# Kernel tuning notes

Measured on AMD Instinct MI355X. Metric: run time of the kernel, lower is better.

The kernel has to match this reference:

```python
import jax, jax.numpy as jnp
import numpy as np

ALPHA = 20.0 / 100.0  # dt / tau


def setup_inputs() -> dict:
    key = jax.random.key(0)
    ks = jax.random.split(key, 5)
    T, B, I, N = 1000, 256, 128, 512
    return {
        "x": jax.random.normal(ks[0], (T, B, I), dtype=jnp.float32),
        "h0": jax.random.normal(ks[1], (B, N), dtype=jnp.float32) * 0.3,
        "W_in": jax.random.normal(ks[2], (N, I), dtype=jnp.float32) / np.sqrt(I),
        "b_in": jax.random.normal(ks[3], (N,), dtype=jnp.float32) * 0.01,
        "W_hh": jax.random.normal(ks[4], (N, N), dtype=jnp.float32) / np.sqrt(N),
    }


def reference(x, h0, W_in, b_in, W_hh):
    # Precompute input projection for all steps in one GEMM: [T,B,N]
    xproj = jnp.einsum("tbi,ni->tbn", x, W_in) + b_in

    def step(h, xp_t):
        h_new = jnp.tanh(xp_t + h @ W_hh.T)
        h = h * (1.0 - ALPHA) + h_new * ALPHA
        return h, h

    hidden, output = jax.lax.scan(step, h0, xproj)
    return output, hidden
```

## Files before the change

### kernel.cpp

```cpp
#include <hip/hip_runtime.h>
#include <hip/hip_bf16.h>


typedef __bf16 bf16;
typedef __bf16 bf16x8 __attribute__((ext_vector_type(8)));
typedef float floatx4 __attribute__((ext_vector_type(4)));
typedef unsigned short u16;
typedef u16 u16x4 __attribute__((ext_vector_type(4)));

#define T_STEPS 1000
#define BATCH 256
#define NDIM 512
#define IDIM 128

__global__ void pack_kernel(const float* __restrict__ W_hh,
                            const float* __restrict__ W_in,
                            bf16x8* __restrict__ Whpack,
                            bf16x8* __restrict__ WinHi,
                            bf16x8* __restrict__ WinLo) {
    int e = blockIdx.x * 256 + threadIdx.x;
    if (e < 32768) {
        int g = e >> 10, s = (e >> 6) & 15, lane = e & 63;
        int n = 16 * g + (lane & 15);
        int k = 32 * s + 8 * (lane >> 4);
        const float* src = W_hh + n * 512 + k;
        bf16x8 v;
#pragma unroll
        for (int j = 0; j < 8; j++) v[j] = (bf16)src[j];
        Whpack[e] = v;
    } else {
        int e2 = e - 32768;
        if (e2 < 8192) {
            int g = e2 >> 8, s = (e2 >> 6) & 3, lane = e2 & 63;
            int n = 16 * g + (lane & 15);
            int i = 32 * s + 8 * (lane >> 4);
            const float* src = W_in + n * 128 + i;
            bf16x8 vh, vl;
#pragma unroll
            for (int j = 0; j < 8; j++) {
                float w = src[j];
                bf16 h = (bf16)w;
                vh[j] = h;
                vl[j] = (bf16)(w - (float)h);
            }
            WinHi[e2] = vh;
            WinLo[e2] = vl;
        }
    }
}

__global__ __launch_bounds__(256)
void xproj_kernel(const float* __restrict__ x,
                  const float* __restrict__ b_in,
                  const bf16x8* __restrict__ WinHi,
                  const bf16x8* __restrict__ WinLo,
                  float* __restrict__ out) {
    __shared__ float stg[4][2][16 * 36];
    const int wave = threadIdx.x >> 6, lane = threadIdx.x & 63;
    const int m = lane & 15, q = lane >> 4;
    const long tile0 = ((long)blockIdx.x * 4 + wave) * 2;

    bf16x8 ah[2][4], al[2][4];
#pragma unroll
    for (int tt = 0; tt < 2; tt++) {
        const floatx4* xr = (const floatx4*)(x + ((tile0 + tt) * 16 + m) * IDIM);
#pragma unroll
        for (int s = 0; s < 4; s++) {
            floatx4 w0 = xr[s * 8 + q * 2];
            floatx4 w1 = xr[s * 8 + q * 2 + 1];
#pragma unroll
            for (int j = 0; j < 4; j++) {
                float a0 = w0[j], a1 = w1[j];
                bf16 h0 = (bf16)a0, h1 = (bf16)a1;
                ah[tt][s][j] = h0;
                ah[tt][s][j + 4] = h1;
                al[tt][s][j] = (bf16)(a0 - (float)h0);
                al[tt][s][j + 4] = (bf16)(a1 - (float)h1);
            }
        }
    }

    const int rrow = lane >> 3;
    const int rcol = (lane & 7) * 4;

#pragma unroll 2
    for (int gp = 0; gp < 16; gp++) {
        floatx4 acc[2][2];
#pragma unroll
        for (int tt = 0; tt < 2; tt++)
#pragma unroll
            for (int p = 0; p < 2; p++) acc[tt][p] = (floatx4){0.f, 0.f, 0.f, 0.f};

#pragma unroll
        for (int s = 0; s < 4; s++) {
            bf16x8 bh0 = WinHi[((2 * gp) * 4 + s) * 64 + lane];
            bf16x8 bl0 = WinLo[((2 * gp) * 4 + s) * 64 + lane];
            bf16x8 bh1 = WinHi[((2 * gp + 1) * 4 + s) * 64 + lane];
            bf16x8 bl1 = WinLo[((2 * gp + 1) * 4 + s) * 64 + lane];
#pragma unroll
            for (int tt = 0; tt < 2; tt++) {
                acc[tt][0] = __builtin_amdgcn_mfma_f32_16x16x32_bf16(ah[tt][s], bh0, acc[tt][0], 0, 0, 0);
                acc[tt][0] = __builtin_amdgcn_mfma_f32_16x16x32_bf16(al[tt][s], bh0, acc[tt][0], 0, 0, 0);
                acc[tt][0] = __builtin_amdgcn_mfma_f32_16x16x32_bf16(ah[tt][s], bl0, acc[tt][0], 0, 0, 0);
                acc[tt][1] = __builtin_amdgcn_mfma_f32_16x16x32_bf16(ah[tt][s], bh1, acc[tt][1], 0, 0, 0);
                acc[tt][1] = __builtin_amdgcn_mfma_f32_16x16x32_bf16(al[tt][s], bh1, acc[tt][1], 0, 0, 0);
                acc[tt][1] = __builtin_amdgcn_mfma_f32_16x16x32_bf16(ah[tt][s], bl1, acc[tt][1], 0, 0, 0);
            }
        }
        float b0v = b_in[16 * (2 * gp) + m];
        float b1v = b_in[16 * (2 * gp + 1) + m];
#pragma unroll
        for (int tt = 0; tt < 2; tt++) {
            float* T = stg[wave][tt];
#pragma unroll
            for (int r = 0; r < 4; r++) {
                T[(q * 4 + r) * 36 + m] = acc[tt][0][r] + b0v;
                T[(q * 4 + r) * 36 + 16 + m] = acc[tt][1][r] + b1v;
            }
        }
#pragma unroll
        for (int tt = 0; tt < 2; tt++) {
            const float* T = stg[wave][tt];
            long r0 = (tile0 + tt) * 16;
#pragma unroll
            for (int k = 0; k < 2; k++) {
                int row = k * 8 + rrow;
                floatx4 v = *(const floatx4*)(T + row * 36 + rcol);
                *(floatx4*)(out + (r0 + row) * NDIM + 32 * gp + rcol) = v;
            }
        }
    }
}

__global__ __launch_bounds__(512, 2)
void scan_kernel(const float* __restrict__ h0,
                 const bf16x8* __restrict__ Whpack,
                 float* __restrict__ out) {
    extern __shared__ char smem[];
    bf16x8* Wlds = (bf16x8*)smem;
    bf16x8* pack = (bf16x8*)(smem + 128 * 1024);

    const int tid = threadIdx.x;
    const int wave = tid >> 6, lane = tid & 63;
    const int m = lane & 15, q = lane >> 4;
    const int b0 = blockIdx.x * 16;

    bf16x8 Wr[3][16];
    {
        const bf16x8* base = Whpack + (4 * wave) * 1024 + lane;
#pragma unroll
        for (int i = 0; i < 3; i++)
#pragma unroll
            for (int s = 0; s < 16; s++)
                Wr[i][s] = base[(i * 16 + s) * 64];
    }
    for (int r = 0; r < 16; r++) {
        int e = r * 512 + tid;
        int slot = e >> 10;
        int rem = e & 1023;
        Wlds[e] = Whpack[(4 * slot + 3) * 1024 + rem];
    }
    floatx4 h32[4];
#pragma unroll
    for (int i = 0; i < 4; i++) {
        int n0 = (4 * wave + i) * 16 + q * 4;
        h32[i] = *(const floatx4*)(h0 + (b0 + m) * NDIM + n0);
    }
    for (int e = tid; e < 1024; e += 512) {
        int s = e >> 6, l = e & 63;
        const float* src = h0 + (b0 + (l & 15)) * NDIM + s * 32 + 8 * (l >> 4);
        bf16x8 v;
#pragma unroll
        for (int j = 0; j < 8; j++) v[j] = (bf16)src[j];
        pack[e] = v;
    }
    __syncthreads();

    const int wslot = wave * 1024;

#pragma unroll 1
    for (int t = 0; t < T_STEPS; t++) {
        float* row = out + ((long)(t * BATCH + b0 + m)) * NDIM;
        floatx4 xp[4];
#pragma unroll
        for (int i = 0; i < 4; i++) {
            int n0 = (4 * wave + i) * 16 + q * 4;
            xp[i] = *(const floatx4*)(row + n0);
        }

        floatx4 acc[4];
#pragma unroll
        for (int i = 0; i < 4; i++) acc[i] = (floatx4){0.f, 0.f, 0.f, 0.f};

#pragma unroll
        for (int s = 0; s < 16; s++) {
            bf16x8 hfrag = pack[s * 64 + lane];
#pragma unroll
            for (int i = 0; i < 3; i++)
                acc[i] = __builtin_amdgcn_mfma_f32_16x16x32_bf16(Wr[i][s], hfrag, acc[i], 0, 0, 0);
            bf16x8 wl = Wlds[wslot + s * 64 + lane];
            acc[3] = __builtin_amdgcn_mfma_f32_16x16x32_bf16(wl, hfrag, acc[3], 0, 0, 0);
        }
        asm volatile("s_waitcnt lgkmcnt(0)" ::: "memory");
        __builtin_amdgcn_s_barrier();
        asm volatile("" ::: "memory");

#pragma unroll
        for (int i = 0; i < 4; i++) {
            int n0 = (4 * wave + i) * 16 + q * 4;
            floatx4 z = xp[i] + acc[i];
            floatx4 hn;
#pragma unroll
            for (int r = 0; r < 4; r++) {
                float e = __builtin_amdgcn_exp2f(z[r] * 2.885390081777927f);
                hn[r] = 1.0f - 2.0f * __builtin_amdgcn_rcpf(e + 1.0f);
            }
            h32[i] = h32[i] * 0.8f + hn * 0.2f;
            int sp = n0 >> 5;
            int o = (n0 >> 3) & 3;
            u16x4 pw;
#pragma unroll
            for (int r = 0; r < 4; r++) {
                bf16 hb = (bf16)h32[i][r];
                pw[r] = __builtin_bit_cast(u16, hb);
            }
            *(u16x4*)(((char*)pack) + (sp * 64 + m + 16 * o) * 16 + (n0 & 7) * 2) = pw;
        }
        asm volatile("s_waitcnt lgkmcnt(0)" ::: "memory");
        __builtin_amdgcn_s_barrier();
        asm volatile("" ::: "memory");

#pragma unroll
        for (int i = 0; i < 4; i++) {
            int n0 = (4 * wave + i) * 16 + q * 4;
            __builtin_nontemporal_store(h32[i], (floatx4*)(row + n0));
        }
    }

    float* hid = out + (long)T_STEPS * BATCH * NDIM;
#pragma unroll
    for (int i = 0; i < 4; i++) {
        int n0 = (4 * wave + i) * 16 + q * 4;
        *(floatx4*)(hid + (b0 + m) * NDIM + n0) = h32[i];
    }
}

extern "C" void kernel_launch(void* const* d_in, const int* in_sizes, int n_in,
                              void* d_out, int out_size, void* d_ws, size_t ws_size,
                              hipStream_t stream) {
    const float* x    = (const float*)d_in[0];
    const float* h0   = (const float*)d_in[1];
    const float* W_in = (const float*)d_in[2];
    const float* b_in = (const float*)d_in[3];
    const float* W_hh = (const float*)d_in[4];
    float* out = (float*)d_out;

    bf16x8* Whpack = (bf16x8*)d_ws;
    bf16x8* WinHi  = (bf16x8*)((char*)d_ws + 524288);
    bf16x8* WinLo  = (bf16x8*)((char*)d_ws + 655360);

    hipFuncSetAttribute((const void*)scan_kernel,
                        hipFuncAttributeMaxDynamicSharedMemorySize, 147456);

    pack_kernel<<<160, 256, 0, stream>>>(W_hh, W_in, Whpack, WinHi, WinLo);
    xproj_kernel<<<2000, 256, 0, stream>>>(x, b_in, WinHi, WinLo, out);
    scan_kernel<<<16, 512, 147456, stream>>>(h0, Whpack, out);
}
```

Measured before the change: 4.180 ms.

## Double-buffer packed hidden state to remove one barrier per scan step

Splits the bf16 hidden-state pack in LDS into two ping-pong buffers, so each step reads the current buffer and writes the next. This needs only a single barrier per step instead of two. The tanh and leaky-update arithmetic is folded into one expression, and the output store now happens inline as a regular store rather than nontemporal after a barrier. LDS use grows to 160KB, and the time loop is unrolled by two steps.

```diff
diff --git a/kernel.cpp b/kernel.cpp
--- a/kernel.cpp
+++ b/kernel.cpp
@@ -138,7 +138,8 @@
                  float* __restrict__ out) {
     extern __shared__ char smem[];
     bf16x8* Wlds = (bf16x8*)smem;
-    bf16x8* pack = (bf16x8*)(smem + 128 * 1024);
+    bf16x8* pk0  = (bf16x8*)(smem + 131072);
+    bf16x8* pk1  = (bf16x8*)(smem + 147456);
 
     const int tid = threadIdx.x;
     const int wave = tid >> 6, lane = tid & 63;
@@ -172,14 +173,13 @@
         bf16x8 v;
 #pragma unroll
         for (int j = 0; j < 8; j++) v[j] = (bf16)src[j];
-        pack[e] = v;
+        pk0[e] = v;
     }
     __syncthreads();
 
     const int wslot = wave * 1024;
 
-#pragma unroll 1
-    for (int t = 0; t < T_STEPS; t++) {
+    auto step = [&](int t, const bf16x8* pcur, bf16x8* pnxt) {
         float* row = out + ((long)(t * BATCH + b0 + m)) * NDIM;
         floatx4 xp[4];
 #pragma unroll
@@ -194,28 +194,25 @@
 
 #pragma unroll
         for (int s = 0; s < 16; s++) {
-            bf16x8 hfrag = pack[s * 64 + lane];
+            bf16x8 hfrag = pcur[s * 64 + lane];
 #pragma unroll
             for (int i = 0; i < 3; i++)
                 acc[i] = __builtin_amdgcn_mfma_f32_16x16x32_bf16(Wr[i][s], hfrag, acc[i], 0, 0, 0);
             bf16x8 wl = Wlds[wslot + s * 64 + lane];
             acc[3] = __builtin_amdgcn_mfma_f32_16x16x32_bf16(wl, hfrag, acc[3], 0, 0, 0);
         }
-        asm volatile("s_waitcnt lgkmcnt(0)" ::: "memory");
-        __builtin_amdgcn_s_barrier();
-        asm volatile("" ::: "memory");
 
 #pragma unroll
         for (int i = 0; i < 4; i++) {
             int n0 = (4 * wave + i) * 16 + q * 4;
             floatx4 z = xp[i] + acc[i];
-            floatx4 hn;
 #pragma unroll
             for (int r = 0; r < 4; r++) {
                 float e = __builtin_amdgcn_exp2f(z[r] * 2.885390081777927f);
-                hn[r] = 1.0f - 2.0f * __builtin_amdgcn_rcpf(e + 1.0f);
-            }
-            h32[i] = h32[i] * 0.8f + hn * 0.2f;
+                float rc = __builtin_amdgcn_rcpf(e + 1.0f);
+                h32[i][r] = h32[i][r] * 0.8f + 0.2f - 0.4f * rc;
+            }
+            *(floatx4*)(row + n0) = h32[i];
             int sp = n0 >> 5;
             int o = (n0 >> 3) & 3;
             u16x4 pw;
@@ -224,17 +221,15 @@
                 bf16 hb = (bf16)h32[i][r];
                 pw[r] = __builtin_bit_cast(u16, hb);
             }
-            *(u16x4*)(((char*)pack) + (sp * 64 + m + 16 * o) * 16 + (n0 & 7) * 2) = pw;
-        }
-        asm volatile("s_waitcnt lgkmcnt(0)" ::: "memory");
-        __builtin_amdgcn_s_barrier();
-        asm volatile("" ::: "memory");
-
-#pragma unroll
-        for (int i = 0; i < 4; i++) {
-            int n0 = (4 * wave + i) * 16 + q * 4;
-            __builtin_nontemporal_store(h32[i], (floatx4*)(row + n0));
-        }
+            *(u16x4*)(((char*)pnxt) + (sp * 64 + m + 16 * o) * 16 + (n0 & 7) * 2) = pw;
+        }
+        __syncthreads();
+    };
+
+#pragma unroll 1
+    for (int t = 0; t < T_STEPS; t += 2) {
+        step(t, pk0, pk1);
+        step(t + 1, pk1, pk0);
     }
 
     float* hid = out + (long)T_STEPS * BATCH * NDIM;
@@ -260,9 +255,9 @@
     bf16x8* WinLo  = (bf16x8*)((char*)d_ws + 655360);
 
     hipFuncSetAttribute((const void*)scan_kernel,
-                        hipFuncAttributeMaxDynamicSharedMemorySize, 147456);
+                        hipFuncAttributeMaxDynamicSharedMemorySize, 163840);
 
     pack_kernel<<<160, 256, 0, stream>>>(W_hh, W_in, Whpack, WinHi, WinLo);
     xproj_kernel<<<2000, 256, 0, stream>>>(x, b_in, WinHi, WinLo, out);
-    scan_kernel<<<16, 512, 147456, stream>>>(h0, Whpack, out);
-}
+    scan_kernel<<<16, 512, 163840, stream>>>(h0, Whpack, out);
+}
```

New measurement: 4.261 ms. No clear change (+1.9%).
